# Optimization experiments

Measured on AMD Instinct MI355X. Metric: run time of the kernel, lower is better.

Reference implementation:

```python
import jax, jax.numpy as jnp
import numpy as np

N_GROUPS = 8
TOPK_GROUPS = 4
TOPK = 8
ROUTE_SCALE = 2.5


def setup_inputs() -> dict:
    key = jax.random.key(0)
    k1, k2 = jax.random.split(key)
    x = jax.random.normal(k1, (16384, 7168), dtype=jnp.float32)
    weight = jax.random.normal(k2, (256, 7168), dtype=jnp.float32) * 0.02
    return {"x": x, "weight": weight}


def reference(x, weight):
    # scores: [T, E]
    scores = jax.nn.sigmoid(jnp.einsum("td,ed->te", x, weight))
    original_scores = scores
    T = x.shape[0]
    # group-limited routing: [T, G, E/G]
    g = scores.reshape(T, N_GROUPS, -1)
    group_scores = g.max(axis=-1)                       # [T, G]
    _, gidx = jax.lax.top_k(group_scores, TOPK_GROUPS)  # [T, topk_groups]
    keep = jnp.zeros((T, N_GROUPS), bool).at[jnp.arange(T)[:, None], gidx].set(True)
    masked = jnp.where(keep[:, :, None], g, -jnp.inf).reshape(T, -1)  # [T, E]
    _, indices = jax.lax.top_k(masked, TOPK)            # [T, topk]
    weights = jnp.take_along_axis(original_scores, indices, axis=1)
    # sigmoid score_func: normalize over selected experts
    weights = weights / weights.sum(axis=-1, keepdims=True)
    weights = weights * ROUTE_SCALE
    return weights.astype(x.dtype), indices
```

## Files before the change

kernel.cpp:

```cpp
#include <hip/hip_runtime.h>
#include <math.h>

constexpr int T  = 16384;
constexpr int D  = 7168;
constexpr int E  = 256;
constexpr int NG = 8;
constexpr int GS = 32;
constexpr int TOPK_G = 4;
constexpr int TOPK   = 8;

constexpr int BM = 32;
constexpr int BK = 16;
constexpr int NT = 256;

constexpr int AS_S = 36;
constexpr int BS_S = 260;
constexpr int SC_S = 257;

__global__ __launch_bounds__(NT, 2)
void gate_fused(const float* __restrict__ X, const float* __restrict__ W,
                float* __restrict__ out) {
    __shared__ float As[BK * AS_S];
    __shared__ float Bs[BK * BS_S];
    __shared__ float Sc[BM * SC_S];

    const int tid  = threadIdx.x;
    const int row0 = blockIdx.x * BM;

    const int lrow = tid >> 2;
    const int kq4  = (tid & 3) << 2;
    const bool a_loader = (tid < 128);

    const float* aptr = X + (size_t)(row0 + (lrow & 31)) * D + kq4;
    const float* bptr = W + (size_t)lrow * D + kq4;

    const int ty = tid >> 5;
    const int tx = tid & 31;

    float acc[4][8];
#pragma unroll
    for (int i = 0; i < 4; ++i)
#pragma unroll
        for (int j = 0; j < 8; ++j) acc[i][j] = 0.0f;

    float4 areg;
    if (a_loader) areg = *(const float4*)aptr;
    float4 breg0 = *(const float4*)(bptr);
    float4 breg1 = *(const float4*)(bptr + (size_t)64  * D);
    float4 breg2 = *(const float4*)(bptr + (size_t)128 * D);
    float4 breg3 = *(const float4*)(bptr + (size_t)192 * D);
    aptr += BK; bptr += BK;

    constexpr int NKT = D / BK;
    for (int kt = 0; kt < NKT; ++kt) {
        __syncthreads();
        {
            const float* b0 = (const float*)&breg0;
            const float* b1 = (const float*)&breg1;
            const float* b2 = (const float*)&breg2;
            const float* b3 = (const float*)&breg3;
#pragma unroll
            for (int j = 0; j < 4; ++j) {
                Bs[(kq4 + j) * BS_S + lrow]        = b0[j];
                Bs[(kq4 + j) * BS_S + 64  + lrow]  = b1[j];
                Bs[(kq4 + j) * BS_S + 128 + lrow]  = b2[j];
                Bs[(kq4 + j) * BS_S + 192 + lrow]  = b3[j];
            }
            if (a_loader) {
                const float* a = (const float*)&areg;
#pragma unroll
                for (int j = 0; j < 4; ++j)
                    As[(kq4 + j) * AS_S + (lrow & 31)] = a[j];
            }
        }
        __syncthreads();
        if (kt + 1 < NKT) {
            if (a_loader) areg = *(const float4*)aptr;
            breg0 = *(const float4*)(bptr);
            breg1 = *(const float4*)(bptr + (size_t)64  * D);
            breg2 = *(const float4*)(bptr + (size_t)128 * D);
            breg3 = *(const float4*)(bptr + (size_t)192 * D);
            aptr += BK; bptr += BK;
        }

        float c2[4][8];
#pragma unroll
        for (int k = 0; k < BK; ++k) {
            float af[4], bf[8];
            *(float4*)&af[0] = *(const float4*)&As[k * AS_S + (ty << 2)];
            *(float4*)&bf[0] = *(const float4*)&Bs[k * BS_S + (tx << 2)];
            *(float4*)&bf[4] = *(const float4*)&Bs[k * BS_S + 128 + (tx << 2)];
#pragma unroll
            for (int i = 0; i < 4; ++i)
#pragma unroll
                for (int j = 0; j < 8; ++j) {
                    if (k == 0) c2[i][j]  = af[i] * bf[j];
                    else        c2[i][j] += af[i] * bf[j];
                }
        }
#pragma unroll
        for (int i = 0; i < 4; ++i)
#pragma unroll
            for (int j = 0; j < 8; ++j) acc[i][j] += c2[i][j];
    }

    __syncthreads();
#pragma unroll
    for (int i = 0; i < 4; ++i) {
        const int r = (ty << 2) + i;
#pragma unroll
        for (int j = 0; j < 8; ++j) {
            const int c = (j < 4) ? ((tx << 2) + j) : (128 + (tx << 2) + j - 4);
            Sc[r * SC_S + c] = acc[i][j];
        }
    }
    __syncthreads();

    if (tid < BM) {
        float* sc = &Sc[tid * SC_S];
        for (int e = 0; e < E; ++e) {
            const float v = sc[e];
            sc[e] = 1.0f / (1.0f + expf(-v));
        }
        float gmax[NG];
#pragma unroll
        for (int g = 0; g < NG; ++g) {
            float m = -INFINITY;
            for (int j = 0; j < GS; ++j) m = fmaxf(m, sc[g * GS + j]);
            gmax[g] = m;
        }
        int cmask = 0;
#pragma unroll
        for (int it = 0; it < TOPK_G; ++it) {
            float best = -INFINITY; int bg = 0;
#pragma unroll
            for (int g = 0; g < NG; ++g) {
                const bool free_g = ((cmask >> g) & 1) == 0;
                if (free_g && gmax[g] > best) { best = gmax[g]; bg = g; }
            }
            cmask |= (1 << bg);
        }
#pragma unroll
        for (int g = 0; g < NG; ++g) {
            if (((cmask >> g) & 1) == 0) {
                for (int j = 0; j < GS; ++j) sc[g * GS + j] = -INFINITY;
            }
        }
        float vals[TOPK]; int idxs[TOPK];
        for (int it = 0; it < TOPK; ++it) {
            float best = -INFINITY; int bi = 0;
            for (int e = 0; e < E; ++e) {
                const float v = sc[e];
                if (v > best) { best = v; bi = e; }
            }
            vals[it] = best; idxs[it] = bi;
            sc[bi] = -INFINITY;
        }
        float s = 0.0f;
#pragma unroll
        for (int k = 0; k < TOPK; ++k) s += vals[k];
        const float scale = 2.5f / s;

        float* ow = out + (size_t)(row0 + tid) * TOPK;
        float* oi = out + (size_t)T * TOPK + (size_t)(row0 + tid) * TOPK;
#pragma unroll
        for (int k = 0; k < TOPK; ++k) {
            ow[k] = vals[k] * scale;
            oi[k] = (float)idxs[k];
        }
    }
}

extern "C" void kernel_launch(void* const* d_in, const int* in_sizes, int n_in,
                              void* d_out, int out_size, void* d_ws, size_t ws_size,
                              hipStream_t stream) {
    const float* x = (const float*)d_in[0];
    const float* w = (const float*)d_in[1];
    float* out = (float*)d_out;
    (void)in_sizes; (void)n_in; (void)out_size; (void)d_ws; (void)ws_size;
    gate_fused<<<dim3(T / BM), dim3(NT), 0, stream>>>(x, w, out);
}
```

Before: 1.421 ms.

## Use split-fp16 MFMA for gate GEMM with fp32 fixup for near-tie rows

Replaces the scalar fp32 FMA GEMM with MFMA 32x32x16 fp16 instructions. Both X and the pre-scaled weight are split into high and low fp16 parts, and three products are summed to approximate fp32 accuracy. The weight is repacked into an MFMA-friendly layout by a separate kernel on every call. Rows whose top-k selection has a small score gap are flagged through an atomic list and recomputed exactly in fp32 by a fixup kernel. This adds extra launches, a workspace dependency and a packing pass, and it relies on the gap heuristic to keep the routing choices correct.

After: 1.369 ms. -3.6%, faster.

```diff
diff --git a/kernel.cpp b/kernel.cpp
--- a/kernel.cpp
+++ b/kernel.cpp
@@ -1,5 +1,10 @@
 #include <hip/hip_runtime.h>
 #include <math.h>
+
+typedef _Float16 f16;
+typedef f16  f16x4  __attribute__((ext_vector_type(4)));
+typedef f16  f16x8  __attribute__((ext_vector_type(8)));
+typedef float f32x16 __attribute__((ext_vector_type(16)));
 
 constexpr int T  = 16384;
 constexpr int D  = 7168;
@@ -9,33 +14,273 @@
 constexpr int TOPK_G = 4;
 constexpr int TOPK   = 8;
 
-constexpr int BM = 32;
-constexpr int BK = 16;
-constexpr int NT = 256;
-
-constexpr int AS_S = 36;
-constexpr int BS_S = 260;
-constexpr int SC_S = 257;
-
-__global__ __launch_bounds__(NT, 2)
-void gate_fused(const float* __restrict__ X, const float* __restrict__ W,
-                float* __restrict__ out) {
+constexpr float W_SCALE     = 256.0f;
+constexpr float INV_W_SCALE = 1.0f / 256.0f;
+constexpr float EPS_GAP     = 2e-5f;
+
+constexpr size_t WS_CNT    = 0;
+constexpr size_t WS_LIST   = 64;
+constexpr size_t WS_BPACK  = 131072;
+constexpr size_t BPACK_ELEMS = (size_t)448 * 8 * 2 * 512;
+constexpr size_t WS_NEEDED = WS_BPACK + BPACK_ELEMS * sizeof(f16);
+
+__device__ float route_row(float* sc, float* ow, float* oi) {
+    float gmax[NG];
+#pragma unroll
+    for (int g = 0; g < NG; ++g) {
+        float m = sc[g * GS];
+        for (int j = 1; j < GS; ++j) m = fmaxf(m, sc[g * GS + j]);
+        gmax[g] = m;
+    }
+    int cmask = 0;
+    float top5[5];
+#pragma unroll
+    for (int it = 0; it < 5; ++it) {
+        float best = -INFINITY; int bg = 0;
+#pragma unroll
+        for (int g = 0; g < NG; ++g) {
+            if (!((cmask >> g) & 1) && gmax[g] > best) { best = gmax[g]; bg = g; }
+        }
+        top5[it] = best;
+        if (it < TOPK_G) cmask |= (1 << bg);
+    }
+    const float gap45 = top5[3] - top5[4];
+#pragma unroll
+    for (int g = 0; g < NG; ++g) {
+        if (!((cmask >> g) & 1)) {
+            for (int j = 0; j < GS; ++j) sc[g * GS + j] = -INFINITY;
+        }
+    }
+    float vals[TOPK + 1]; int idxs[TOPK + 1];
+    for (int it = 0; it < TOPK + 1; ++it) {
+        float best = -INFINITY; int bi = 0;
+        for (int e = 0; e < E; ++e) {
+            const float v = sc[e];
+            if (v > best) { best = v; bi = e; }
+        }
+        vals[it] = best; idxs[it] = bi; sc[bi] = -INFINITY;
+    }
+    float mingap = gap45;
+#pragma unroll
+    for (int i = 0; i < TOPK; ++i) mingap = fminf(mingap, vals[i] - vals[i + 1]);
+
+    float s = 0.0f;
+#pragma unroll
+    for (int k = 0; k < TOPK; ++k) s += vals[k];
+    const float scale = 2.5f / s;
+#pragma unroll
+    for (int k = 0; k < TOPK; ++k) { ow[k] = vals[k] * scale; oi[k] = (float)idxs[k]; }
+    return mingap;
+}
+
+__global__ void zero_cnt(int* c) { if (threadIdx.x == 0) *c = 0; }
+
+__global__ __launch_bounds__(256)
+void pack_w(const float* __restrict__ W, f16* __restrict__ Bp) {
+    const int gid  = blockIdx.x * 256 + threadIdx.x;
+    const int lane = gid & 63;
+    const int f    = gid >> 6;
+    const int k16  = f >> 3;
+    const int tn   = f & 7;
+    const int e    = tn * 32 + (lane & 31);
+    const int kb   = k16 * 16 + (lane >> 5) * 8;
+    const float* wp = W + (size_t)e * D + kb;
+    const float4 v0 = *(const float4*)wp;
+    const float4 v1 = *(const float4*)(wp + 4);
+    float vv[8] = {v0.x, v0.y, v0.z, v0.w, v1.x, v1.y, v1.z, v1.w};
+    f16x8 h, l;
+#pragma unroll
+    for (int j = 0; j < 8; ++j) {
+        const float s = vv[j] * W_SCALE;
+        const f16 hh = (f16)s;
+        h[j] = hh;
+        l[j] = (f16)(s - (float)hh);
+    }
+    f16* dst = Bp + (size_t)f * 1024 + lane * 8;
+    *(f16x8*)dst         = h;
+    *(f16x8*)(dst + 512) = l;
+}
+
+__global__ __launch_bounds__(512, 2)
+void gate_mfma(const float* __restrict__ X, const f16* __restrict__ Bp,
+               float* __restrict__ out, int* __restrict__ cnt, int* __restrict__ list) {
+    __shared__ f16 Ahl[2][2][2][2][64][8];
+    __shared__ float Sc[64 * 257];
+
+    const int tid  = threadIdx.x;
+    const int lane = tid & 63;
+    const int wv   = tid >> 6;
+    const int row0 = blockIdx.x * 64;
+
+    const int srow  = tid >> 3;
+    const int sq    = tid & 7;
+    const int s_kh  = sq >> 2;
+    const int s_ks  = (sq & 3) * 4;
+    const int s_lane = (srow & 31) + ((s_ks >> 3) << 5);
+    const int s_j   = s_ks & 7;
+    const int s_tile = srow >> 5;
+
+    const float* xp = X + (size_t)(row0 + srow) * D + sq * 4;
+
+    const f16* bptr = Bp + (size_t)wv * 1024 + (size_t)lane * 8;
+
+    f32x16 acc0, acc1;
+#pragma unroll
+    for (int r = 0; r < 16; ++r) { acc0[r] = 0.0f; acc1[r] = 0.0f; }
+
+    float4 xv = *(const float4*)xp; xp += 32;
+    f16x8 bh0 = *(const f16x8*)(bptr + 0);
+    f16x8 bl0 = *(const f16x8*)(bptr + 512);
+    f16x8 bh1 = *(const f16x8*)(bptr + 8192);
+    f16x8 bl1 = *(const f16x8*)(bptr + 8704);
+    bptr += 16384;
+
+    {
+        f16x4 h, l;
+        const float* v = (const float*)&xv;
+#pragma unroll
+        for (int u = 0; u < 4; ++u) {
+            const f16 hh = (f16)v[u];
+            h[u] = hh; l[u] = (f16)(v[u] - (float)hh);
+        }
+        *(f16x4*)&Ahl[0][s_kh][s_tile][0][s_lane][s_j] = h;
+        *(f16x4*)&Ahl[0][s_kh][s_tile][1][s_lane][s_j] = l;
+    }
+    __syncthreads();
+
+    constexpr int NCH = D / 32;
+    int buf = 0;
+    for (int c = 0; c < NCH; ++c) {
+        const bool has_next = (c + 1 < NCH);
+        float4 xn;
+        f16x8 nbh0, nbl0, nbh1, nbl1;
+        if (has_next) {
+            xn   = *(const float4*)xp; xp += 32;
+            nbh0 = *(const f16x8*)(bptr + 0);
+            nbl0 = *(const f16x8*)(bptr + 512);
+            nbh1 = *(const f16x8*)(bptr + 8192);
+            nbl1 = *(const f16x8*)(bptr + 8704);
+            bptr += 16384;
+        }
+        {
+            const f16x8 a0h = *(const f16x8*)&Ahl[buf][0][0][0][lane][0];
+            const f16x8 a0l = *(const f16x8*)&Ahl[buf][0][0][1][lane][0];
+            const f16x8 a1h = *(const f16x8*)&Ahl[buf][0][1][0][lane][0];
+            const f16x8 a1l = *(const f16x8*)&Ahl[buf][0][1][1][lane][0];
+            acc0 = __builtin_amdgcn_mfma_f32_32x32x16_f16(a0h, bh0, acc0, 0, 0, 0);
+            acc1 = __builtin_amdgcn_mfma_f32_32x32x16_f16(a1h, bh0, acc1, 0, 0, 0);
+            acc0 = __builtin_amdgcn_mfma_f32_32x32x16_f16(a0h, bl0, acc0, 0, 0, 0);
+            acc1 = __builtin_amdgcn_mfma_f32_32x32x16_f16(a1h, bl0, acc1, 0, 0, 0);
+            acc0 = __builtin_amdgcn_mfma_f32_32x32x16_f16(a0l, bh0, acc0, 0, 0, 0);
+            acc1 = __builtin_amdgcn_mfma_f32_32x32x16_f16(a1l, bh0, acc1, 0, 0, 0);
+        }
+        {
+            const f16x8 a0h = *(const f16x8*)&Ahl[buf][1][0][0][lane][0];
+            const f16x8 a0l = *(const f16x8*)&Ahl[buf][1][0][1][lane][0];
+            const f16x8 a1h = *(const f16x8*)&Ahl[buf][1][1][0][lane][0];
+            const f16x8 a1l = *(const f16x8*)&Ahl[buf][1][1][1][lane][0];
+            acc0 = __builtin_amdgcn_mfma_f32_32x32x16_f16(a0h, bh1, acc0, 0, 0, 0);
+            acc1 = __builtin_amdgcn_mfma_f32_32x32x16_f16(a1h, bh1, acc1, 0, 0, 0);
+            acc0 = __builtin_amdgcn_mfma_f32_32x32x16_f16(a0h, bl1, acc0, 0, 0, 0);
+            acc1 = __builtin_amdgcn_mfma_f32_32x32x16_f16(a1h, bl1, acc1, 0, 0, 0);
+            acc0 = __builtin_amdgcn_mfma_f32_32x32x16_f16(a0l, bh1, acc0, 0, 0, 0);
+            acc1 = __builtin_amdgcn_mfma_f32_32x32x16_f16(a1l, bh1, acc1, 0, 0, 0);
+        }
+        if (has_next) {
+            f16x4 h, l;
+            const float* v = (const float*)&xn;
+#pragma unroll
+            for (int u = 0; u < 4; ++u) {
+                const f16 hh = (f16)v[u];
+                h[u] = hh; l[u] = (f16)(v[u] - (float)hh);
+            }
+            *(f16x4*)&Ahl[buf ^ 1][s_kh][s_tile][0][s_lane][s_j] = h;
+            *(f16x4*)&Ahl[buf ^ 1][s_kh][s_tile][1][s_lane][s_j] = l;
+            bh0 = nbh0; bl0 = nbl0; bh1 = nbh1; bl1 = nbl1;
+        }
+        __syncthreads();
+        buf ^= 1;
+    }
+
+    const int ccol  = wv * 32 + (lane & 31);
+    const int rbase = 4 * (lane >> 5);
+#pragma unroll
+    for (int r = 0; r < 16; ++r) {
+        const int rw = (r & 3) + 8 * (r >> 2) + rbase;
+        Sc[rw * 257 + ccol]        = acc0[r];
+        Sc[(rw + 32) * 257 + ccol] = acc1[r];
+    }
+    __syncthreads();
+
+    if (tid < 64) {
+        float* sc = &Sc[tid * 257];
+        for (int e = 0; e < E; ++e)
+            sc[e] = 1.0f / (1.0f + expf(-sc[e] * INV_W_SCALE));
+        const int token = row0 + tid;
+        const float mingap = route_row(sc, out + (size_t)token * TOPK,
+                                       out + (size_t)T * TOPK + (size_t)token * TOPK);
+        if (mingap < EPS_GAP) {
+            const int s = atomicAdd(cnt, 1);
+            if (s < T) list[s] = token;
+        }
+    }
+}
+
+__global__ __launch_bounds__(256)
+void gate_fixup(const float* __restrict__ X, const float* __restrict__ W,
+                float* __restrict__ out, const int* __restrict__ cnt,
+                const int* __restrict__ list) {
+    __shared__ float xs[D];
+    __shared__ float sc[E];
+    int n = *cnt; if (n > T) n = T;
+    for (int i = blockIdx.x; i < n; i += gridDim.x) {
+        __syncthreads();
+        const int tok = list[i];
+        const float* xr = X + (size_t)tok * D;
+#pragma unroll
+        for (int s = 0; s < D / (256 * 4); ++s) {
+            const int q = s * 256 + threadIdx.x;
+            *(float4*)&xs[q * 4] = *(const float4*)&xr[q * 4];
+        }
+        __syncthreads();
+        const float* wr = W + (size_t)threadIdx.x * D;
+        float acc = 0.0f;
+        for (int c0 = 0; c0 < D; c0 += 64) {
+            float c2 = 0.0f;
+#pragma unroll
+            for (int k = 0; k < 64; k += 4) {
+                const float4 wv = *(const float4*)&wr[c0 + k];
+                const float4 xv = *(const float4*)&xs[c0 + k];
+                c2 += xv.x * wv.x + xv.y * wv.y + xv.z * wv.z + xv.w * wv.w;
+            }
+            acc += c2;
+        }
+        sc[threadIdx.x] = 1.0f / (1.0f + expf(-acc));
+        __syncthreads();
+        if (threadIdx.x == 0) {
+            route_row(sc, out + (size_t)tok * TOPK,
+                      out + (size_t)T * TOPK + (size_t)tok * TOPK);
+        }
+    }
+}
+
+__global__ __launch_bounds__(256, 2)
+void gate_fused_fp32(const float* __restrict__ X, const float* __restrict__ W,
+                     float* __restrict__ out) {
+    constexpr int BM = 32, BK = 16, AS_S = 36, BS_S = 260, SC_S = 257;
     __shared__ float As[BK * AS_S];
     __shared__ float Bs[BK * BS_S];
     __shared__ float Sc[BM * SC_S];
 
     const int tid  = threadIdx.x;
     const int row0 = blockIdx.x * BM;
-
     const int lrow = tid >> 2;
     const int kq4  = (tid & 3) << 2;
     const bool a_loader = (tid < 128);
 
     const float* aptr = X + (size_t)(row0 + (lrow & 31)) * D + kq4;
     const float* bptr = W + (size_t)lrow * D + kq4;
-
-    const int ty = tid >> 5;
-    const int tx = tid & 31;
+    const int ty = tid >> 5, tx = tid & 31;
 
     float acc[4][8];
 #pragma unroll
@@ -46,7 +291,7 @@
     float4 areg;
     if (a_loader) areg = *(const float4*)aptr;
     float4 breg0 = *(const float4*)(bptr);
-    float4 breg1 = *(const float4*)(bptr + (size_t)64  * D);
+    float4 breg1 = *(const float4*)(bptr + (size_t)64 * D);
     float4 breg2 = *(const float4*)(bptr + (size_t)128 * D);
     float4 breg3 = *(const float4*)(bptr + (size_t)192 * D);
     aptr += BK; bptr += BK;
@@ -61,10 +306,10 @@
             const float* b3 = (const float*)&breg3;
 #pragma unroll
             for (int j = 0; j < 4; ++j) {
-                Bs[(kq4 + j) * BS_S + lrow]        = b0[j];
-                Bs[(kq4 + j) * BS_S + 64  + lrow]  = b1[j];
-                Bs[(kq4 + j) * BS_S + 128 + lrow]  = b2[j];
-                Bs[(kq4 + j) * BS_S + 192 + lrow]  = b3[j];
+                Bs[(kq4 + j) * BS_S + lrow]       = b0[j];
+                Bs[(kq4 + j) * BS_S + 64 + lrow]  = b1[j];
+                Bs[(kq4 + j) * BS_S + 128 + lrow] = b2[j];
+                Bs[(kq4 + j) * BS_S + 192 + lrow] = b3[j];
             }
             if (a_loader) {
                 const float* a = (const float*)&areg;
@@ -77,12 +322,11 @@
         if (kt + 1 < NKT) {
             if (a_loader) areg = *(const float4*)aptr;
             breg0 = *(const float4*)(bptr);
-            breg1 = *(const float4*)(bptr + (size_t)64  * D);
+            breg1 = *(const float4*)(bptr + (size_t)64 * D);
             breg2 = *(const float4*)(bptr + (size_t)128 * D);
             breg3 = *(const float4*)(bptr + (size_t)192 * D);
             aptr += BK; bptr += BK;
         }
-
         float c2[4][8];
 #pragma unroll
         for (int k = 0; k < BK; ++k) {
@@ -94,7 +338,7 @@
             for (int i = 0; i < 4; ++i)
 #pragma unroll
                 for (int j = 0; j < 8; ++j) {
-                    if (k == 0) c2[i][j]  = af[i] * bf[j];
+                    if (k == 0) c2[i][j] = af[i] * bf[j];
                     else        c2[i][j] += af[i] * bf[j];
                 }
         }
@@ -118,56 +362,10 @@
 
     if (tid < BM) {
         float* sc = &Sc[tid * SC_S];
-        for (int e = 0; e < E; ++e) {
-            const float v = sc[e];
-            sc[e] = 1.0f / (1.0f + expf(-v));
-        }
-        float gmax[NG];
-#pragma unroll
-        for (int g = 0; g < NG; ++g) {
-            float m = -INFINITY;
-            for (int j = 0; j < GS; ++j) m = fmaxf(m, sc[g * GS + j]);
-            gmax[g] = m;
-        }
-        int cmask = 0;
-#pragma unroll
-        for (int it = 0; it < TOPK_G; ++it) {
-            float best = -INFINITY; int bg = 0;
-#pragma unroll
-            for (int g = 0; g < NG; ++g) {
-                const bool free_g = ((cmask >> g) & 1) == 0;
-                if (free_g && gmax[g] > best) { best = gmax[g]; bg = g; }
-            }
-            cmask |= (1 << bg);
-        }
-#pragma unroll
-        for (int g = 0; g < NG; ++g) {
-            if (((cmask >> g) & 1) == 0) {
-                for (int j = 0; j < GS; ++j) sc[g * GS + j] = -INFINITY;
-            }
-        }
-        float vals[TOPK]; int idxs[TOPK];
-        for (int it = 0; it < TOPK; ++it) {
-            float best = -INFINITY; int bi = 0;
-            for (int e = 0; e < E; ++e) {
-                const float v = sc[e];
-                if (v > best) { best = v; bi = e; }
-            }
-            vals[it] = best; idxs[it] = bi;
-            sc[bi] = -INFINITY;
-        }
-        float s = 0.0f;
-#pragma unroll
-        for (int k = 0; k < TOPK; ++k) s += vals[k];
-        const float scale = 2.5f / s;
-
-        float* ow = out + (size_t)(row0 + tid) * TOPK;
-        float* oi = out + (size_t)T * TOPK + (size_t)(row0 + tid) * TOPK;
-#pragma unroll
-        for (int k = 0; k < TOPK; ++k) {
-            ow[k] = vals[k] * scale;
-            oi[k] = (float)idxs[k];
-        }
+        for (int e = 0; e < E; ++e) sc[e] = 1.0f / (1.0f + expf(-sc[e]));
+        const int token = row0 + tid;
+        route_row(sc, out + (size_t)token * TOPK,
+                  out + (size_t)T * TOPK + (size_t)token * TOPK);
     }
 }
 
@@ -177,6 +375,17 @@
     const float* x = (const float*)d_in[0];
     const float* w = (const float*)d_in[1];
     float* out = (float*)d_out;
-    (void)in_sizes; (void)n_in; (void)out_size; (void)d_ws; (void)ws_size;
-    gate_fused<<<dim3(T / BM), dim3(NT), 0, stream>>>(x, w, out);
-}
+    (void)in_sizes; (void)n_in; (void)out_size;
+
+    if (ws_size >= WS_NEEDED) {
+        int* cnt   = (int*)((char*)d_ws + WS_CNT);
+        int* list  = (int*)((char*)d_ws + WS_LIST);
+        f16* bpack = (f16*)((char*)d_ws + WS_BPACK);
+        zero_cnt<<<1, 64, 0, stream>>>(cnt);
+        pack_w<<<896, 256, 0, stream>>>(w, bpack);
+        gate_mfma<<<T / 64, 512, 0, stream>>>(x, bpack, out, cnt, list);
+        gate_fixup<<<256, 256, 0, stream>>>(x, w, out, cnt, list);
+    } else {
+        gate_fused_fp32<<<T / 32, 256, 0, stream>>>(x, w, out);
+    }
+}
```
